# Performance work log

Measured on AMD Instinct MI355X. Metric: run time of the kernel, lower is better.

Reference implementation:

```python
import jax, jax.numpy as jnp
import numpy as np

B, T, C = 512, 512, 96


def setup_inputs() -> dict:
    key = jax.random.key(0)
    k1, k2, k3, k4, k5 = jax.random.split(key, 5)
    emissions = jax.random.normal(k1, (B, T, C), dtype=jnp.float32)
    tags = jax.random.randint(k2, (B, T), 0, C, dtype=jnp.int64)
    mask = jnp.ones((B, T), dtype=jnp.int32)
    transitions = jax.random.normal(k3, (C, C), dtype=jnp.float32)
    start_transitions = jax.random.normal(k4, (C,), dtype=jnp.float32)
    end_transitions = jax.random.normal(k5, (C,), dtype=jnp.float32)
    return {
        "emissions": emissions,
        "tags": tags,
        "mask": mask,
        "transitions": transitions,
        "start_transitions": start_transitions,
        "end_transitions": end_transitions,
    }


def _log_partition(emissions, mask, transitions, start_transitions, end_transitions):
    # forward algorithm: carry log_prob [B, C] over T-1 steps via scan
    log_prob0 = start_transitions + emissions[:, 0]  # [B, C]
    em_rest = jnp.swapaxes(emissions[:, 1:], 0, 1)   # [T-1, B, C]
    mk_rest = jnp.swapaxes(mask[:, 1:], 0, 1).astype(bool)  # [T-1, B]

    def step(log_prob, xs):
        emit_t, mask_t = xs
        # score[b, i, j] = log_prob[b, i] + transitions[i, j] + emit_t[b, j]
        score = log_prob[:, :, None] + transitions[None, :, :] + emit_t[:, None, :]
        log_prob_next = jax.nn.logsumexp(score, axis=1)  # [B, C]
        return jnp.where(mask_t[:, None], log_prob_next, log_prob), None

    log_prob, _ = jax.lax.scan(step, log_prob0, (em_rest, mk_rest))
    return jax.nn.logsumexp(log_prob + end_transitions, axis=1)  # [B]


def _joint_likelihood(emissions, tags, mask, transitions, start_transitions, end_transitions):
    # emission score of the gold tag at each step: [B, T]
    emit = jnp.take_along_axis(emissions, tags[:, :, None], axis=2)[..., 0]
    # transition score between consecutive gold tags: [B, T-1]
    trans = transitions[tags[:, :-1], tags[:, 1:]]
    m = mask[:, 1:].astype(emissions.dtype)
    last_idx = jnp.sum(mask, axis=1).astype(jnp.int32) - 1  # [B]
    last_tag = jnp.take_along_axis(tags, last_idx[:, None].astype(tags.dtype), axis=1)[:, 0]
    score = (start_transitions[tags[:, 0]] + emit[:, 0]
             + jnp.sum(m * (trans + emit[:, 1:]), axis=1)
             + end_transitions[last_tag])
    return score  # [B]


def reference(emissions, tags, mask, transitions, start_transitions, end_transitions):
    log_den = _log_partition(emissions, mask, transitions, start_transitions, end_transitions)
    log_num = _joint_likelihood(emissions, tags, mask, transitions, start_transitions, end_transitions)
    return jnp.mean(log_den - log_num)
```

## Files before the change

### kernel.cpp

```cpp
#include <hip/hip_runtime.h>
#include <math.h>

#define CC 96
#define BB 512
#define TT 512

__global__ __launch_bounds__(128) void crf_prep(const float* __restrict__ trans,
                                                float* __restrict__ E,
                                                float* __restrict__ maxT) {
    int j = threadIdx.x;
    if (j < CC) {
        float m = -INFINITY;
        for (int i = 0; i < CC; ++i) m = fmaxf(m, trans[i * CC + j]);
        maxT[j] = m;
        for (int i = 0; i < CC; ++i) E[i * CC + j] = __expf(trans[i * CC + j] - m);
    }
}

__global__ __launch_bounds__(64) void pack_mask(const int* __restrict__ mask,
                                                unsigned* __restrict__ mbits) {
    const int b = blockIdx.x;
    const int w = threadIdx.x;
    if (w < 16) {
        unsigned bits = 0u;
        for (int k = 0; k < 32; ++k)
            bits |= (mask[b * TT + w * 32 + k] ? 1u : 0u) << k;
        mbits[b * 16 + w] = bits;
    }
}

#define PKFMA_LO(A_, S_, E_) \
    asm("v_pk_fma_f32 %0, %1, %2, %0 op_sel:[0,0,0] op_sel_hi:[0,1,1]" \
        : "+v"(A_) : "v"(S_), "v"(E_))
#define PKFMA_HI(A_, S_, E_) \
    asm("v_pk_fma_f32 %0, %1, %2, %0 op_sel:[1,0,0] op_sel_hi:[1,1,1]" \
        : "+v"(A_) : "v"(S_), "v"(E_))

#define FSTEP(PF_, K_, BIT_, REN_) do {                                       \
    const int sl_ = (K_) & 3;                                                 \
    const int pr_ = (K_) & 1;                                                 \
    const float2 ce_ = es[sl_];                                               \
    es[sl_] = *(const float2*)(PF_);                                          \
    const float scx_ = __expf(mTx + ce_.x);                                   \
    const float scy_ = __expf(mTy + ce_.y);                                   \
    float2 a0={0.f,0.f}, a1={0.f,0.f}, a2={0.f,0.f}, a3={0.f,0.f};            \
    _Pragma("unroll")                                                         \
    for (int k_ = 0; k_ < 24; k_ += 4) {                                      \
        const float2 p0_ = *(const float2*)&pb[w][pr_][k_];                   \
        const float2 p1_ = *(const float2*)&pb[w][pr_][k_ + 2];               \
        PKFMA_LO(a0, p0_, ep2[k_]);                                           \
        PKFMA_HI(a1, p0_, ep2[k_ + 1]);                                       \
        PKFMA_LO(a2, p1_, ep2[k_ + 2]);                                       \
        PKFMA_HI(a3, p1_, ep2[k_ + 3]);                                       \
    }                                                                         \
    float2 mine_;                                                             \
    mine_.x = (a0.x + a1.x) + (a2.x + a3.x);                                  \
    mine_.y = (a0.y + a1.y) + (a2.y + a3.y);                                  \
    if (act) *(float2*)&pex[w][pr_][2 * l] = mine_;                           \
    asm volatile("s_waitcnt lgkmcnt(0)" ::: "memory");                        \
    __builtin_amdgcn_s_barrier();                                             \
    const float2 o0_ = *(const float2*)&pex[0][pr_][2 * lc];                  \
    const float2 o1_ = *(const float2*)&pex[1][pr_][2 * lc];                  \
    const float2 o2_ = *(const float2*)&pex[2][pr_][2 * lc];                  \
    const float2 o3_ = *(const float2*)&pex[3][pr_][2 * lc];                  \
    const float qx_ = (o0_.x + o1_.x) + (o2_.x + o3_.x);                      \
    const float qy_ = (o0_.y + o1_.y) + (o2_.y + o3_.y);                      \
    if (BIT_) { px = qx_ * scx_; py = qy_ * scy_; }                           \
    if (REN_) {                                                               \
        float r_ = px + py;                                                   \
        _Pragma("unroll")                                                     \
        for (int o_ = 32; o_; o_ >>= 1) r_ += __shfl_xor(r_, o_);             \
        const float inv_ = 1.0f / r_;                                         \
        px *= inv_; py *= inv_;                                               \
        S += (double)__logf(r_);                                              \
    }                                                                         \
    if (l >= wlo && l < whi)                                                  \
        *(float2*)&pb[w][pr_ ^ 1][2 * l - 24 * w] = make_float2(px, py);      \
} while (0)

#define BSTEP(PF_, SL_, PR_, BIT_, REN_) do {                                 \
    const float2 ce_ = es[SL_];                                               \
    es[SL_] = *(const float2*)(PF_);                                          \
    float2 a0={0.f,0.f}, a1={0.f,0.f}, a2={0.f,0.f}, a3={0.f,0.f};            \
    _Pragma("unroll")                                                         \
    for (int k_ = 0; k_ < 24; k_ += 4) {                                      \
        const float2 u0_ = *(const float2*)&pb[w][PR_][k_];                   \
        const float2 u1_ = *(const float2*)&pb[w][PR_][k_ + 2];               \
        PKFMA_LO(a0, u0_, eb2[k_]);                                           \
        PKFMA_HI(a1, u0_, eb2[k_ + 1]);                                       \
        PKFMA_LO(a2, u1_, eb2[k_ + 2]);                                       \
        PKFMA_HI(a3, u1_, eb2[k_ + 3]);                                       \
    }                                                                         \
    float2 mine_;                                                             \
    mine_.x = (a0.x + a1.x) + (a2.x + a3.x);                                  \
    mine_.y = (a0.y + a1.y) + (a2.y + a3.y);                                  \
    if (act) *(float2*)&pex[w][PR_][2 * l] = mine_;                           \
    asm volatile("s_waitcnt lgkmcnt(0)" ::: "memory");                        \
    __builtin_amdgcn_s_barrier();                                             \
    const float2 o0_ = *(const float2*)&pex[0][PR_][2 * lc];                  \
    const float2 o1_ = *(const float2*)&pex[1][PR_][2 * lc];                  \
    const float2 o2_ = *(const float2*)&pex[2][PR_][2 * lc];                  \
    const float2 o3_ = *(const float2*)&pex[3][PR_][2 * lc];                  \
    const float qx_ = (o0_.x + o1_.x) + (o2_.x + o3_.x);                      \
    const float qy_ = (o0_.y + o1_.y) + (o2_.y + o3_.y);                      \
    if (act && (BIT_)) { cx = qx_; cy = qy_; }                                \
    if (REN_) {                                                               \
        float r_ = cx + cy;                                                   \
        _Pragma("unroll")                                                     \
        for (int o_ = 32; o_; o_ >>= 1) r_ += __shfl_xor(r_, o_);             \
        const float inv_ = 1.0f / r_;                                         \
        cx *= inv_; cy *= inv_;                                               \
        S += (double)__logf(r_);                                              \
    }                                                                         \
    if (l >= wlo && l < whi)                                                  \
        *(float2*)&pb[w][(PR_) ^ 1][2 * l - 24 * w] =                         \
            make_float2(__expf(mTx + ce_.x) * cx, __expf(mTy + ce_.y) * cy);  \
} while (0)

__global__ __launch_bounds__(256, 4)
void crf_half(const float* __restrict__ emissions,
              const unsigned* __restrict__ mbits,
              const float* __restrict__ start_t,
              const float* __restrict__ end_t,
              const float* __restrict__ E,
              const float* __restrict__ maxT,
              float* __restrict__ pmid, float* __restrict__ cmid,
              double* __restrict__ Sf, double* __restrict__ Sb) {
    const int dir = blockIdx.x >> 9;
    const int b = blockIdx.x & 511;
    const int w = threadIdx.x >> 6;
    const int l = threadIdx.x & 63;
    const bool act = (l < 48);
    const int lc = act ? l : 47;
    const int s0 = 2 * lc;
    const int wlo = 12 * w, whi = 12 * w + 12;

    __shared__ __align__(16) float pb[4][2][24];
    __shared__ __align__(16) float pex[4][2][CC];

    const float* ep = emissions + (size_t)b * TT * CC + s0;
    const float mTx = act ? maxT[s0]     : -INFINITY;
    const float mTy = act ? maxT[s0 + 1] : -INFINITY;
    double S = 0.0;
    float2 es[4];

    if (dir == 0) {
        float2 ep2[24];
#pragma unroll
        for (int k = 0; k < 24; ++k)
            ep2[k] = *(const float2*)(E + (size_t)(24 * w + k) * CC + s0);

        float px = 0.f, py = 0.f;
        {
            const float2 e0 = *(const float2*)ep;
            if (act) {
                px = __expf(start_t[s0]     + e0.x);
                py = __expf(start_t[s0 + 1] + e0.y);
            }
        }
        if (l >= wlo && l < whi)
            *(float2*)&pb[w][1][2 * l - 24 * w] = make_float2(px, py);

#pragma unroll
        for (int s = 1; s <= 4; ++s) es[s & 3] = *(const float2*)(ep + (size_t)s * CC);
        const float* pf = ep + (size_t)5 * CC;

        const unsigned wb0 = mbits[b * 16];
#pragma unroll
        for (int k = 1; k < 8; ++k) {
            FSTEP(pf, k, (wb0 >> k) & 1u, 0);
            pf += CC;
        }
        unsigned swc = wb0 >> 8;
        for (int sb = 1; sb < 32; ++sb) {
            const int sbn = sb + 1;
            const unsigned swn = mbits[b * 16 + (sbn >> 2)] >> ((sbn & 3) * 8);
#pragma unroll
            for (int k = 0; k < 8; ++k) {
                FSTEP(pf, k, (swc >> k) & 1u, k == 0);
                pf += CC;
            }
            swc = swn;
        }
        if (w == 0 && act) *(float2*)&pmid[(size_t)b * CC + s0] = make_float2(px, py);
        if (w == 0 && l == 0) Sf[b] = S;
    } else {
        float2 eb2[24];
#pragma unroll
        for (int k = 0; k < 24; ++k)
            eb2[k] = make_float2(E[(size_t)s0 * CC + 24 * w + k],
                                 E[(size_t)(s0 + 1) * CC + 24 * w + k]);

        float cx = act ? __expf(end_t[s0])     : 0.f;
        float cy = act ? __expf(end_t[s0 + 1]) : 0.f;
        {
            const float2 e511 = *(const float2*)(ep + (size_t)511 * CC);
            if (l >= wlo && l < whi)
                *(float2*)&pb[w][0][2 * l - 24 * w] =
                    make_float2(__expf(mTx + e511.x) * cx, __expf(mTy + e511.y) * cy);
        }
#pragma unroll
        for (int s = 0; s < 4; ++s)
            es[(510 - s) & 3] = *(const float2*)(ep + (size_t)(510 - s) * CC);
        const float* pf = ep + (size_t)506 * CC;

        unsigned wv = mbits[b * 16 + 15] >> 24;
        for (int grp = 63; grp >= 32; --grp) {
            const int gn = grp - 1;
            const unsigned wn = mbits[b * 16 + (gn >> 2)] >> ((gn & 3) * 8);
#pragma unroll
            for (int k = 0; k < 8; ++k) {
                BSTEP(pf, (6 - k) & 3, k & 1, (wv >> (7 - k)) & 1u, k == 7);
                pf -= CC;
            }
            wv = wn;
        }
        if (w == 0 && act) *(float2*)&cmid[(size_t)b * CC + s0] = make_float2(cx, cy);
        if (w == 0 && l == 0) Sb[b] = S;
    }
}

__global__ __launch_bounds__(64) void crf_combine(const float* __restrict__ pmid,
                                                  const float* __restrict__ cmid,
                                                  const double* __restrict__ Sf,
                                                  const double* __restrict__ Sb,
                                                  float* __restrict__ log_den) {
    const int b = blockIdx.x;
    const int l = threadIdx.x;
    float v = 0.f;
    if (l < 48) {
        const float2 p2 = *(const float2*)&pmid[(size_t)b * CC + 2 * l];
        const float2 c2 = *(const float2*)&cmid[(size_t)b * CC + 2 * l];
        v = p2.x * c2.x + p2.y * c2.y;
    }
#pragma unroll
    for (int off = 32; off; off >>= 1) v += __shfl_xor(v, off);
    if (l == 0) log_den[b] = (float)(Sf[b] + Sb[b] + (double)__logf(v));
}

__global__ __launch_bounds__(256) void crf_joint(const float* __restrict__ emissions,
                                                 const int* __restrict__ tags,
                                                 const int* __restrict__ mask,
                                                 const float* __restrict__ trans,
                                                 const float* __restrict__ start_t,
                                                 const float* __restrict__ end_t,
                                                 float* __restrict__ log_num) {
    const int b = blockIdx.x;
    const int tid = threadIdx.x;
    float s = 0.f;
    int mcount = 0;
    for (int t = tid; t < TT; t += 256) {
        int tg = tags[b * TT + t];
        float em = emissions[((size_t)b * TT + t) * CC + tg];
        int mk = mask[b * TT + t];
        mcount += mk;
        if (t == 0) {
            s += start_t[tg] + em;
        } else {
            int tp = tags[b * TT + t - 1];
            s += mk ? (trans[tp * CC + tg] + em) : 0.f;
        }
    }
    __shared__ float sred[4];
    __shared__ int mred[4];
#pragma unroll
    for (int off = 32; off; off >>= 1) {
        s += __shfl_xor(s, off);
        mcount += __shfl_xor(mcount, off);
    }
    if ((tid & 63) == 0) { sred[tid >> 6] = s; mred[tid >> 6] = mcount; }
    __syncthreads();
    if (tid == 0) {
        float tot = (sred[0] + sred[1]) + (sred[2] + sred[3]);
        int mt = (mred[0] + mred[1]) + (mred[2] + mred[3]);
        int last_tag = tags[b * TT + (mt - 1)];
        log_num[b] = tot + end_t[last_tag];
    }
}

__global__ __launch_bounds__(512) void crf_final(const float* __restrict__ log_den,
                                                 const float* __restrict__ log_num,
                                                 float* __restrict__ out) {
    const int tid = threadIdx.x;
    float d = log_den[tid] - log_num[tid];
#pragma unroll
    for (int off = 32; off; off >>= 1) d += __shfl_xor(d, off);
    __shared__ float sred[8];
    if ((tid & 63) == 0) sred[tid >> 6] = d;
    __syncthreads();
    if (tid == 0) {
        float tot = 0.f;
        for (int w = 0; w < 8; ++w) tot += sred[w];
        out[0] = tot / (float)BB;
    }
}

extern "C" void kernel_launch(void* const* d_in, const int* in_sizes, int n_in,
                              void* d_out, int out_size, void* d_ws, size_t ws_size,
                              hipStream_t stream) {
    const float* emissions = (const float*)d_in[0];
    const int*   tags      = (const int*)d_in[1];
    const int*   mask      = (const int*)d_in[2];
    const float* trans     = (const float*)d_in[3];
    const float* start_t   = (const float*)d_in[4];
    const float* end_t     = (const float*)d_in[5];
    float* out = (float*)d_out;

    float*    ws      = (float*)d_ws;
    float*    E       = ws;
    float*    maxT    = ws + 9216;
    float*    log_den = ws + 9312;
    float*    log_num = ws + 9824;
    unsigned* mbits   = (unsigned*)(ws + 10336);
    float*    pmid    = ws + 18528;
    float*    cmid    = ws + 67680;
    double*   Sf      = (double*)(ws + 116832);
    double*   Sb      = (double*)(ws + 117856);

    crf_prep<<<1, 128, 0, stream>>>(trans, E, maxT);
    pack_mask<<<BB, 64, 0, stream>>>(mask, mbits);
    crf_half<<<2 * BB, 256, 0, stream>>>(emissions, mbits, start_t, end_t, E, maxT,
                                         pmid, cmid, Sf, Sb);
    crf_combine<<<BB, 64, 0, stream>>>(pmid, cmid, Sf, Sb, log_den);
    crf_joint<<<BB, 256, 0, stream>>>(emissions, tags, mask, trans, start_t, end_t, log_num);
    crf_final<<<1, 512, 0, stream>>>(log_den, log_num, out);
}
```

Measured before the change: 179.5 us.

## Split CRF matvec across lane quads with DPP reduction, one barrier per step

```diff
diff --git a/kernel.cpp b/kernel.cpp
--- a/kernel.cpp
+++ b/kernel.cpp
@@ -36,6 +36,41 @@
     asm("v_pk_fma_f32 %0, %1, %2, %0 op_sel:[1,0,0] op_sel_hi:[1,1,1]" \
         : "+v"(A_) : "v"(S_), "v"(E_))
 
+__device__ __forceinline__ float quad_add(float v) {
+    int t = __builtin_amdgcn_update_dpp(0, __float_as_int(v), 0xB1, 0xF, 0xF, true);
+    v += __int_as_float(t);
+    t = __builtin_amdgcn_update_dpp(0, __float_as_int(v), 0x4E, 0xF, 0xF, true);
+    return v + __int_as_float(t);
+}
+
+#define QMATVEC(PR_, ER_)                                                     \
+    float2 a0={0.f,0.f}, a1={0.f,0.f}, a2={0.f,0.f}, a3={0.f,0.f};            \
+    _Pragma("unroll")                                                         \
+    for (int k_ = 0; k_ < 24; k_ += 4) {                                      \
+        const float2 p0_ = *(const float2*)&pb[PR_][rb + k_];                 \
+        const float2 p1_ = *(const float2*)&pb[PR_][rb + k_ + 2];             \
+        PKFMA_LO(a0, p0_, ER_[k_]);                                           \
+        PKFMA_HI(a1, p0_, ER_[k_ + 1]);                                       \
+        PKFMA_LO(a2, p1_, ER_[k_ + 2]);                                       \
+        PKFMA_HI(a3, p1_, ER_[k_ + 3]);                                       \
+    }                                                                         \
+    const float qx_ = quad_add((a0.x + a1.x) + (a2.x + a3.x));                \
+    const float qy_ = quad_add((a0.y + a1.y) + (a2.y + a3.y));
+
+#define RENORM_BLOCK(PX_, PY_)                                                \
+    {                                                                         \
+        float loc_ = (g == 0) ? (PX_ + PY_) : 0.f;                            \
+        _Pragma("unroll")                                                     \
+        for (int o_ = 32; o_; o_ >>= 1) loc_ += __shfl_xor(loc_, o_);         \
+        if (l == 0) wsum[v] = loc_;                                           \
+        asm volatile("s_waitcnt lgkmcnt(0)" ::: "memory");                    \
+        __builtin_amdgcn_s_barrier();                                         \
+        const float r_ = (wsum[0] + wsum[1]) + wsum[2];                       \
+        const float inv_ = 1.0f / r_;                                         \
+        PX_ *= inv_; PY_ *= inv_;                                             \
+        S += (double)__logf(r_);                                              \
+    }
+
 #define FSTEP(PF_, K_, BIT_, REN_) do {                                       \
     const int sl_ = (K_) & 3;                                                 \
     const int pr_ = (K_) & 1;                                                 \
@@ -43,81 +78,31 @@
     es[sl_] = *(const float2*)(PF_);                                          \
     const float scx_ = __expf(mTx + ce_.x);                                   \
     const float scy_ = __expf(mTy + ce_.y);                                   \
-    float2 a0={0.f,0.f}, a1={0.f,0.f}, a2={0.f,0.f}, a3={0.f,0.f};            \
-    _Pragma("unroll")                                                         \
-    for (int k_ = 0; k_ < 24; k_ += 4) {                                      \
-        const float2 p0_ = *(const float2*)&pb[w][pr_][k_];                   \
-        const float2 p1_ = *(const float2*)&pb[w][pr_][k_ + 2];               \
-        PKFMA_LO(a0, p0_, ep2[k_]);                                           \
-        PKFMA_HI(a1, p0_, ep2[k_ + 1]);                                       \
-        PKFMA_LO(a2, p1_, ep2[k_ + 2]);                                       \
-        PKFMA_HI(a3, p1_, ep2[k_ + 3]);                                       \
-    }                                                                         \
-    float2 mine_;                                                             \
-    mine_.x = (a0.x + a1.x) + (a2.x + a3.x);                                  \
-    mine_.y = (a0.y + a1.y) + (a2.y + a3.y);                                  \
-    if (act) *(float2*)&pex[w][pr_][2 * l] = mine_;                           \
+    __builtin_amdgcn_s_setprio(1);                                            \
+    QMATVEC(pr_, ep2)                                                         \
+    __builtin_amdgcn_s_setprio(0);                                            \
+    if (BIT_) { px = qx_ * scx_; py = qy_ * scy_; }                           \
+    if (REN_) RENORM_BLOCK(px, py)                                            \
+    if (g == 0) *(float2*)&pb[pr_ ^ 1][pidx] = make_float2(px, py);           \
     asm volatile("s_waitcnt lgkmcnt(0)" ::: "memory");                        \
     __builtin_amdgcn_s_barrier();                                             \
-    const float2 o0_ = *(const float2*)&pex[0][pr_][2 * lc];                  \
-    const float2 o1_ = *(const float2*)&pex[1][pr_][2 * lc];                  \
-    const float2 o2_ = *(const float2*)&pex[2][pr_][2 * lc];                  \
-    const float2 o3_ = *(const float2*)&pex[3][pr_][2 * lc];                  \
-    const float qx_ = (o0_.x + o1_.x) + (o2_.x + o3_.x);                      \
-    const float qy_ = (o0_.y + o1_.y) + (o2_.y + o3_.y);                      \
-    if (BIT_) { px = qx_ * scx_; py = qy_ * scy_; }                           \
-    if (REN_) {                                                               \
-        float r_ = px + py;                                                   \
-        _Pragma("unroll")                                                     \
-        for (int o_ = 32; o_; o_ >>= 1) r_ += __shfl_xor(r_, o_);             \
-        const float inv_ = 1.0f / r_;                                         \
-        px *= inv_; py *= inv_;                                               \
-        S += (double)__logf(r_);                                              \
-    }                                                                         \
-    if (l >= wlo && l < whi)                                                  \
-        *(float2*)&pb[w][pr_ ^ 1][2 * l - 24 * w] = make_float2(px, py);      \
 } while (0)
 
 #define BSTEP(PF_, SL_, PR_, BIT_, REN_) do {                                 \
     const float2 ce_ = es[SL_];                                               \
     es[SL_] = *(const float2*)(PF_);                                          \
-    float2 a0={0.f,0.f}, a1={0.f,0.f}, a2={0.f,0.f}, a3={0.f,0.f};            \
-    _Pragma("unroll")                                                         \
-    for (int k_ = 0; k_ < 24; k_ += 4) {                                      \
-        const float2 u0_ = *(const float2*)&pb[w][PR_][k_];                   \
-        const float2 u1_ = *(const float2*)&pb[w][PR_][k_ + 2];               \
-        PKFMA_LO(a0, u0_, eb2[k_]);                                           \
-        PKFMA_HI(a1, u0_, eb2[k_ + 1]);                                       \
-        PKFMA_LO(a2, u1_, eb2[k_ + 2]);                                       \
-        PKFMA_HI(a3, u1_, eb2[k_ + 3]);                                       \
-    }                                                                         \
-    float2 mine_;                                                             \
-    mine_.x = (a0.x + a1.x) + (a2.x + a3.x);                                  \
-    mine_.y = (a0.y + a1.y) + (a2.y + a3.y);                                  \
-    if (act) *(float2*)&pex[w][PR_][2 * l] = mine_;                           \
+    __builtin_amdgcn_s_setprio(1);                                            \
+    QMATVEC(PR_, eb2)                                                         \
+    __builtin_amdgcn_s_setprio(0);                                            \
+    if (BIT_) { cx = qx_; cy = qy_; }                                         \
+    if (REN_) RENORM_BLOCK(cx, cy)                                            \
+    if (g == 0) *(float2*)&pb[(PR_) ^ 1][pidx] =                              \
+        make_float2(__expf(mTx + ce_.x) * cx, __expf(mTy + ce_.y) * cy);      \
     asm volatile("s_waitcnt lgkmcnt(0)" ::: "memory");                        \
     __builtin_amdgcn_s_barrier();                                             \
-    const float2 o0_ = *(const float2*)&pex[0][PR_][2 * lc];                  \
-    const float2 o1_ = *(const float2*)&pex[1][PR_][2 * lc];                  \
-    const float2 o2_ = *(const float2*)&pex[2][PR_][2 * lc];                  \
-    const float2 o3_ = *(const float2*)&pex[3][PR_][2 * lc];                  \
-    const float qx_ = (o0_.x + o1_.x) + (o2_.x + o3_.x);                      \
-    const float qy_ = (o0_.y + o1_.y) + (o2_.y + o3_.y);                      \
-    if (act && (BIT_)) { cx = qx_; cy = qy_; }                                \
-    if (REN_) {                                                               \
-        float r_ = cx + cy;                                                   \
-        _Pragma("unroll")                                                     \
-        for (int o_ = 32; o_; o_ >>= 1) r_ += __shfl_xor(r_, o_);             \
-        const float inv_ = 1.0f / r_;                                         \
-        cx *= inv_; cy *= inv_;                                               \
-        S += (double)__logf(r_);                                              \
-    }                                                                         \
-    if (l >= wlo && l < whi)                                                  \
-        *(float2*)&pb[w][(PR_) ^ 1][2 * l - 24 * w] =                         \
-            make_float2(__expf(mTx + ce_.x) * cx, __expf(mTy + ce_.y) * cy);  \
 } while (0)
 
-__global__ __launch_bounds__(256, 4)
+__global__ __launch_bounds__(192, 1)
 void crf_half(const float* __restrict__ emissions,
               const unsigned* __restrict__ mbits,
               const float* __restrict__ start_t,
@@ -128,19 +113,20 @@
               double* __restrict__ Sf, double* __restrict__ Sb) {
     const int dir = blockIdx.x >> 9;
     const int b = blockIdx.x & 511;
-    const int w = threadIdx.x >> 6;
+    const int v = threadIdx.x >> 6;
     const int l = threadIdx.x & 63;
-    const bool act = (l < 48);
-    const int lc = act ? l : 47;
-    const int s0 = 2 * lc;
-    const int wlo = 12 * w, whi = 12 * w + 12;
-
-    __shared__ __align__(16) float pb[4][2][24];
-    __shared__ __align__(16) float pex[4][2][CC];
+    const int g = l & 3;
+    const int jp = 16 * v + (l >> 2);
+    const int s0 = 2 * jp;
+    const int rb = 26 * g;
+    const int pidx = 26 * (s0 / 24) + (s0 % 24);
+
+    __shared__ __align__(16) float pb[2][104];
+    __shared__ float wsum[3];
 
     const float* ep = emissions + (size_t)b * TT * CC + s0;
-    const float mTx = act ? maxT[s0]     : -INFINITY;
-    const float mTy = act ? maxT[s0 + 1] : -INFINITY;
+    const float mTx = maxT[s0];
+    const float mTy = maxT[s0 + 1];
     double S = 0.0;
     float2 es[4];
 
@@ -148,18 +134,17 @@
         float2 ep2[24];
 #pragma unroll
         for (int k = 0; k < 24; ++k)
-            ep2[k] = *(const float2*)(E + (size_t)(24 * w + k) * CC + s0);
-
-        float px = 0.f, py = 0.f;
+            ep2[k] = *(const float2*)(E + (size_t)(24 * g + k) * CC + s0);
+
+        float px, py;
         {
             const float2 e0 = *(const float2*)ep;
-            if (act) {
-                px = __expf(start_t[s0]     + e0.x);
-                py = __expf(start_t[s0 + 1] + e0.y);
-            }
-        }
-        if (l >= wlo && l < whi)
-            *(float2*)&pb[w][1][2 * l - 24 * w] = make_float2(px, py);
+            px = __expf(start_t[s0]     + e0.x);
+            py = __expf(start_t[s0 + 1] + e0.y);
+        }
+        if (g == 0) *(float2*)&pb[1][pidx] = make_float2(px, py);
+        asm volatile("s_waitcnt lgkmcnt(0)" ::: "memory");
+        __builtin_amdgcn_s_barrier();
 
 #pragma unroll
         for (int s = 1; s <= 4; ++s) es[s & 3] = *(const float2*)(ep + (size_t)s * CC);
@@ -182,23 +167,25 @@
             }
             swc = swn;
         }
-        if (w == 0 && act) *(float2*)&pmid[(size_t)b * CC + s0] = make_float2(px, py);
-        if (w == 0 && l == 0) Sf[b] = S;
+        if (g == 0) *(float2*)&pmid[(size_t)b * CC + s0] = make_float2(px, py);
+        if (threadIdx.x == 0) Sf[b] = S;
     } else {
         float2 eb2[24];
 #pragma unroll
         for (int k = 0; k < 24; ++k)
-            eb2[k] = make_float2(E[(size_t)s0 * CC + 24 * w + k],
-                                 E[(size_t)(s0 + 1) * CC + 24 * w + k]);
-
-        float cx = act ? __expf(end_t[s0])     : 0.f;
-        float cy = act ? __expf(end_t[s0 + 1]) : 0.f;
+            eb2[k] = make_float2(E[(size_t)s0 * CC + 24 * g + k],
+                                 E[(size_t)(s0 + 1) * CC + 24 * g + k]);
+
+        float cx = __expf(end_t[s0]);
+        float cy = __expf(end_t[s0 + 1]);
         {
             const float2 e511 = *(const float2*)(ep + (size_t)511 * CC);
-            if (l >= wlo && l < whi)
-                *(float2*)&pb[w][0][2 * l - 24 * w] =
-                    make_float2(__expf(mTx + e511.x) * cx, __expf(mTy + e511.y) * cy);
-        }
+            if (g == 0) *(float2*)&pb[0][pidx] =
+                make_float2(__expf(mTx + e511.x) * cx, __expf(mTy + e511.y) * cy);
+        }
+        asm volatile("s_waitcnt lgkmcnt(0)" ::: "memory");
+        __builtin_amdgcn_s_barrier();
+
 #pragma unroll
         for (int s = 0; s < 4; ++s)
             es[(510 - s) & 3] = *(const float2*)(ep + (size_t)(510 - s) * CC);
@@ -215,8 +202,8 @@
             }
             wv = wn;
         }
-        if (w == 0 && act) *(float2*)&cmid[(size_t)b * CC + s0] = make_float2(cx, cy);
-        if (w == 0 && l == 0) Sb[b] = S;
+        if (g == 0) *(float2*)&cmid[(size_t)b * CC + s0] = make_float2(cx, cy);
+        if (threadIdx.x == 0) Sb[b] = S;
     }
 }
 
@@ -319,7 +306,7 @@
 
     crf_prep<<<1, 128, 0, stream>>>(trans, E, maxT);
     pack_mask<<<BB, 64, 0, stream>>>(mask, mbits);
-    crf_half<<<2 * BB, 256, 0, stream>>>(emissions, mbits, start_t, end_t, E, maxT,
+    crf_half<<<2 * BB, 192, 0, stream>>>(emissions, mbits, start_t, end_t, E, maxT,
                                          pmid, cmid, Sf, Sb);
     crf_combine<<<BB, 64, 0, stream>>>(pmid, cmid, Sf, Sb, log_den);
     crf_joint<<<BB, 256, 0, stream>>>(emissions, tags, mask, trans, start_t, end_t, log_num);
```

Result: faster. 147.0 us (median of 3 runs) (-18.1%).
